# Performance work log

Hardware: AMD Instinct MI355X
Metric: run time of the kernel (lower is better)

The kernel has to match this reference:

```python
import jax, jax.numpy as jnp
import numpy as np

B, T, V = 8, 64, 25
IN_DIM = 64
HID = 64
D = 3 * HID // 2          # 96, per-node feature dim
OUT = 128
N = B * T * V * 2         # 25600 nodes
E = N * 16                # 409600 edges
LAYERS = 2
EPS = 1e-5


def prelu(x, a):
    return jnp.where(x >= 0, x, a * x)


def grouped_conv1x1(x, w, b, groups=3):
    # x: [B, C, V, T]; w: [O, C//groups]; b: [O]  (1x1 conv, groups=3)
    Bb, C, Vv, Tt = x.shape
    O = w.shape[0]
    xg = x.reshape(Bb, groups, C // groups, Vv, Tt)
    wg = w.reshape(groups, O // groups, C // groups)
    y = jnp.einsum('bgivt,goi->bgovt', xg, wg).reshape(Bb, O, Vv, Tt)
    return y + b[None, :, None, None]


def layer_norm(x, g, b):
    m = jnp.mean(x, axis=-1, keepdims=True)
    v = jnp.mean((x - m) ** 2, axis=-1, keepdims=True)
    return (x - m) / jnp.sqrt(v + EPS) * g + b


def _forward(h, src, dst, tp_w1, tp_b1, tp_a, tp_w2, tp_b2,
             tm_w1, tm_b1, tm_a, tm_w2, tm_b2,
             ln_g, ln_b, bn_g, bn_b, bn_rm, bn_rv, act_a,
             gW1, gb1, ga, gW2, gb2, t2_w, t2_b):
    # posture / motion streams -> [B, 3*in_dim, V, T]
    hp = jnp.transpose(h[:, :, :, 0, :], (0, 3, 2, 1))
    hm = jnp.transpose(h[:, :, :, 1, :], (0, 3, 2, 1))
    hp = grouped_conv1x1(prelu(grouped_conv1x1(hp, tp_w1, tp_b1), tp_a), tp_w2, tp_b2)
    hm = grouped_conv1x1(prelu(grouped_conv1x1(hm, tm_w1, tm_b1), tm_a), tm_w2, tm_b2)
    hp = jnp.transpose(hp, (0, 3, 2, 1))[:, :, :, None, :]  # [B,T,V,1,D]
    hm = jnp.transpose(hm, (0, 3, 2, 1))[:, :, :, None, :]
    x = jnp.concatenate([hp, hm], axis=3).reshape(-1, D)     # [N, D]
    raw = x
    hs, es = [], []
    for i in range(LAYERS):
        def gate(h2, i=i):
            # edge gate MLP: Linear -> PReLU -> Linear -> Tanh (dropout eval = id)
            return jnp.tanh(prelu(h2 @ gW1[i] + gb1[i], ga[i]) @ gW2[i] + gb2[i])
        e = gate(x[dst] * x[src])                            # [E, 1]
        z = jax.ops.segment_sum(x[src] * e, dst, num_segments=N)
        y = layer_norm(z + x, ln_g[i], ln_b[i])
        y = (y - bn_rm[i]) / jnp.sqrt(bn_rv[i] + EPS) * bn_g[i] + bn_b[i]  # BN eval
        x = prelu(y, act_a[i])
        hs.append(x)
        es.append(gate(x[dst] * x[src]))   # torch calls the layer a 2nd time for e
    hcat = jnp.concatenate([raw] + hs, axis=1)               # [N, 3D]
    out = hcat @ t2_w + t2_b                                 # dropout eval = id
    ee = jnp.concatenate(es, axis=0)                         # [2E, 1]
    return out, ee


def setup_inputs() -> dict:
    key = jax.random.key(0)
    ks = jax.random.split(key, 40)
    def nrm(k, shape, s=0.05):
        return jax.random.normal(k, shape, jnp.float32) * s
    d = {}
    d['h'] = jax.random.normal(ks[0], (B, T, V, 2, 3 * IN_DIM), jnp.float32)
    d['src'] = jax.random.randint(ks[1], (E,), 0, N, jnp.int32)
    d['dst'] = jax.random.randint(ks[2], (E,), 0, N, jnp.int32)
    # t1_posture / t1_motion grouped 1x1 convs
    d['tp_w1'] = nrm(ks[3], (3 * HID, IN_DIM)); d['tp_b1'] = nrm(ks[4], (3 * HID,))
    d['tp_a'] = jnp.full((1,), 0.25, jnp.float32)
    d['tp_w2'] = nrm(ks[5], (D, HID)); d['tp_b2'] = nrm(ks[6], (D,))
    d['tm_w1'] = nrm(ks[7], (3 * HID, IN_DIM)); d['tm_b1'] = nrm(ks[8], (3 * HID,))
    d['tm_a'] = jnp.full((1,), 0.25, jnp.float32)
    d['tm_w2'] = nrm(ks[9], (D, HID)); d['tm_b2'] = nrm(ks[10], (D,))
    # per-layer norms / activations (stacked over LAYERS)
    d['ln_g'] = jnp.ones((LAYERS, D), jnp.float32); d['ln_b'] = jnp.zeros((LAYERS, D), jnp.float32)
    d['bn_g'] = jnp.ones((LAYERS, D), jnp.float32); d['bn_b'] = jnp.zeros((LAYERS, D), jnp.float32)
    d['bn_rm'] = jnp.zeros((LAYERS, D), jnp.float32); d['bn_rv'] = jnp.ones((LAYERS, D), jnp.float32)
    d['act_a'] = jnp.full((LAYERS,), 0.25, jnp.float32)
    # per-layer FALayer gate MLP
    d['gW1'] = nrm(ks[11], (LAYERS, D, D)); d['gb1'] = nrm(ks[12], (LAYERS, D))
    d['ga'] = jnp.full((LAYERS,), 0.25, jnp.float32)
    d['gW2'] = nrm(ks[13], (LAYERS, D, 1)); d['gb2'] = nrm(ks[14], (LAYERS, 1))
    d['t2_w'] = nrm(ks[15], (3 * D, OUT)); d['t2_b'] = nrm(ks[16], (OUT,))
    return d


def reference(h, src, dst, tp_w1, tp_b1, tp_a, tp_w2, tp_b2,
              tm_w1, tm_b1, tm_a, tm_w2, tm_b2,
              ln_g, ln_b, bn_g, bn_b, bn_rm, bn_rv, act_a,
              gW1, gb1, ga, gW2, gb2, t2_w, t2_b):
    return _forward(h, src, dst, tp_w1, tp_b1, tp_a, tp_w2, tp_b2,
                    tm_w1, tm_b1, tm_a, tm_w2, tm_b2,
                    ln_g, ln_b, bn_g, bn_b, bn_rm, bn_rv, act_a,
                    gW1, gb1, ga, gW2, gb2, t2_w, t2_b)
```

## Files before the change

### kernel.cpp

```cpp
#include <hip/hip_runtime.h>

#define N_NODES 25600
#define N_EDGES 409600
#define EPSV 1e-5f

__device__ __forceinline__ unsigned short f2bf(float f) {
    unsigned int x = __float_as_uint(f);
    x += 0x7fffu + ((x >> 16) & 1u);
    return (unsigned short)(x >> 16);
}
__device__ __forceinline__ unsigned int f2bf2(float a, float b) {
#if __has_builtin(__builtin_amdgcn_cvt_pk_bf16_f32)
    auto r = __builtin_amdgcn_cvt_pk_bf16_f32(a, b);
    unsigned int u;
    __builtin_memcpy(&u, &r, 4);
    return u;
#else
    return (unsigned int)f2bf(a) | ((unsigned int)f2bf(b) << 16);
#endif
}

using frag_ab = __attribute__((ext_vector_type(8))) short;
using frag_cd = __attribute__((ext_vector_type(4))) float;
typedef _Float16 f16x8 __attribute__((ext_vector_type(8)));

#define WST 104
#define TWST 72
#define THST 200

__global__ __launch_bounds__(256) void transform_mfma(
    const float* __restrict__ h,
    const float* __restrict__ tpw1, const float* __restrict__ tpb1, const float* __restrict__ tpa,
    const float* __restrict__ tpw2, const float* __restrict__ tpb2,
    const float* __restrict__ tmw1, const float* __restrict__ tmb1, const float* __restrict__ tma,
    const float* __restrict__ tmw2, const float* __restrict__ tmb2,
    float* __restrict__ xout, _Float16* __restrict__ xh)
{
    __shared__ alignas(16) unsigned short W1s[192 * TWST];
    __shared__ alignas(16) unsigned short W2s[96 * TWST];
    __shared__ alignas(16) unsigned short hs[64 * THST];
    __shared__ float b1s[192];
    __shared__ float b2s[96];

    const int tid = threadIdx.x;
    const int s = blockIdx.y;
    const float* w1 = s ? tmw1 : tpw1;
    const float* b1 = s ? tmb1 : tpb1;
    const float* w2 = s ? tmw2 : tpw2;
    const float* b2 = s ? tmb2 : tpb2;
    const float alpha = (s ? tma : tpa)[0];

    #pragma unroll
    for (int r = 0; r < 12; r++) {
        int idx4 = r * 256 + tid;
        int o = idx4 >> 4, i4 = (idx4 & 15) * 4;
        const float4 a = *(const float4*)&w1[o * 64 + i4];
        *(uint2*)&W1s[o * TWST + i4] = make_uint2(f2bf2(a.x, a.y), f2bf2(a.z, a.w));
    }
    #pragma unroll
    for (int r = 0; r < 6; r++) {
        int idx4 = r * 256 + tid;
        int o = idx4 >> 4, i4 = (idx4 & 15) * 4;
        const float4 a = *(const float4*)&w2[o * 64 + i4];
        *(uint2*)&W2s[o * TWST + i4] = make_uint2(f2bf2(a.x, a.y), f2bf2(a.z, a.w));
    }
    if (tid < 192) b1s[tid] = b1[tid];
    if (tid < 96) b2s[tid] = b2[tid];
    __syncthreads();

    const int lane = tid & 63;
    const int wv = tid >> 6;
    const int quad = lane >> 4;
    const int lcol = lane & 15;
    const int m0 = wv * 16;
    const int j0 = blockIdx.x * 64;

    #pragma unroll
    for (int r = 0; r < 12; r++) {
        int idx = r * 256 + tid;
        int m = idx / 48, q = idx - m * 48;
        const float4 a = *(const float4*)&h[(2 * (j0 + m) + s) * 192 + q * 4];
        *(uint2*)&hs[m * THST + q * 4] = make_uint2(f2bf2(a.x, a.y), f2bf2(a.z, a.w));
    }
    __syncthreads();

    const int arow = (m0 + lcol) * THST;
    #pragma unroll
    for (int g = 0; g < 3; g++) {
        frag_cd acc[4];
        #pragma unroll
        for (int nt = 0; nt < 4; nt++) acc[nt] = (frag_cd){0.f, 0.f, 0.f, 0.f};
        #pragma unroll
        for (int kt = 0; kt < 2; kt++) {
            const int k0 = kt * 32 + quad * 8;
            frag_ab af = *(const frag_ab*)&hs[arow + g * 64 + k0];
            #pragma unroll
            for (int nt = 0; nt < 4; nt++) {
                frag_ab bf = *(const frag_ab*)&W1s[(g * 64 + nt * 16 + lcol) * TWST + k0];
                acc[nt] = __builtin_amdgcn_mfma_f32_16x16x32_bf16(af, bf, acc[nt], 0, 0, 0);
            }
        }
        #pragma unroll
        for (int nt = 0; nt < 4; nt++) {
            const int o = g * 64 + nt * 16 + lcol;
            const float bv = b1s[o];
            #pragma unroll
            for (int reg = 0; reg < 4; reg++) {
                float u = acc[nt][reg] + bv;
                u = u >= 0.f ? u : alpha * u;
                hs[(m0 + quad * 4 + reg) * THST + o] = f2bf(u);
            }
        }
    }
    #pragma unroll
    for (int g2 = 0; g2 < 3; g2++) {
        frag_cd acc[2];
        acc[0] = (frag_cd){0.f, 0.f, 0.f, 0.f};
        acc[1] = (frag_cd){0.f, 0.f, 0.f, 0.f};
        #pragma unroll
        for (int kt = 0; kt < 2; kt++) {
            const int k0 = kt * 32 + quad * 8;
            frag_ab af = *(const frag_ab*)&hs[arow + g2 * 64 + k0];
            #pragma unroll
            for (int nt = 0; nt < 2; nt++) {
                frag_ab bf = *(const frag_ab*)&W2s[(g2 * 32 + nt * 16 + lcol) * TWST + k0];
                acc[nt] = __builtin_amdgcn_mfma_f32_16x16x32_bf16(af, bf, acc[nt], 0, 0, 0);
            }
        }
        #pragma unroll
        for (int nt = 0; nt < 2; nt++) {
            const int o2 = g2 * 32 + nt * 16 + lcol;
            const float bv = b2s[o2];
            #pragma unroll
            for (int reg = 0; reg < 4; reg++) {
                const int node = 2 * (j0 + m0 + quad * 4 + reg) + s;
                const float v = acc[nt][reg] + bv;
                xout[node * 96 + o2] = v;
                xh[node * 96 + o2] = (_Float16)v;
            }
        }
    }
}

template<bool DUAL>
__global__ __launch_bounds__(256) void gate_kernel(
    const _Float16* __restrict__ xh,
    const int* __restrict__ srcp, const int* __restrict__ dstp,
    const int* __restrict__ mapA,
    const float* __restrict__ gW1, const float* __restrict__ gb1,
    const float* __restrict__ ga,  const float* __restrict__ gW2,
    const float* __restrict__ gb2, int layerA, int layerB,
    float* __restrict__ outA, float* __restrict__ outB)
{
    __shared__ alignas(16) _Float16 W1f[(DUAL ? 2 : 1) * 9216];

    const int tid = threadIdx.x;
    {
        const float* W1p = gW1 + layerA * 9216;
        const float* W1q = gW1 + layerB * 9216;
        for (int fi = tid; fi < 1152; fi += 256) {
            int lc = fi & 15, r = fi >> 4;
            int quad = r & 3, t3 = r >> 2;
            int nt = t3 / 3, kt = t3 - nt * 3;
            int n = nt * 16 + lc, k0 = kt * 32 + quad * 8;
            f16x8 v, w;
            #pragma unroll
            for (int j = 0; j < 8; j++) {
                v[j] = (_Float16)W1p[(k0 + j) * 96 + n];
                if (DUAL) w[j] = (_Float16)W1q[(k0 + j) * 96 + n];
            }
            *(f16x8*)&W1f[fi * 8] = v;
            if (DUAL) *(f16x8*)&W1f[9216 + fi * 8] = w;
        }
    }

    const int lane = tid & 63;
    const int wv   = tid >> 6;
    const int quad = lane >> 4;
    const int lcol = lane & 15;
    const int m0   = wv * 16;
    const int erow = m0 + lcol;
    const int koff = quad * 8;

    float w2A[6], b1A[6], w2B[6], b1B[6];
    #pragma unroll
    for (int nt = 0; nt < 6; nt++) {
        w2A[nt] = gW2[layerA * 96 + nt * 16 + lcol];
        b1A[nt] = gb1[layerA * 96 + nt * 16 + lcol];
        if (DUAL) {
            w2B[nt] = gW2[layerB * 96 + nt * 16 + lcol];
            b1B[nt] = gb1[layerB * 96 + nt * 16 + lcol];
        }
    }
    const float alphaA = ga[layerA];
    const float b2A = gb2[layerA];
    const float alphaB = DUAL ? ga[layerB] : 0.f;
    const float b2B = DUAL ? gb2[layerB] : 0.f;

    int si[4], di[4];
    #pragma unroll
    for (int t = 0; t < 4; t++) {
        const int s = blockIdx.x * 256 + t * 64 + erow;
        si[t] = srcp[s];
        di[t] = dstp[s];
    }
    __syncthreads();

    f16x8 A0, A1, A2, B0, B1, B2;
    {
        const _Float16* rs = xh + si[0] * 96 + koff;
        const _Float16* rd = xh + di[0] * 96 + koff;
        A0 = *(const f16x8*)rs;        B0 = *(const f16x8*)rd;
        A1 = *(const f16x8*)(rs + 32); B1 = *(const f16x8*)(rd + 32);
        A2 = *(const f16x8*)(rs + 64); B2 = *(const f16x8*)(rd + 64);
    }

    #pragma unroll
    for (int t = 0; t < 4; t++) {
        f16x8 p0 = A0 * B0;
        f16x8 p1 = A1 * B1;
        f16x8 p2 = A2 * B2;
        if (t < 3) {
            const _Float16* rs = xh + si[t + 1] * 96 + koff;
            const _Float16* rd = xh + di[t + 1] * 96 + koff;
            A0 = *(const f16x8*)rs;        B0 = *(const f16x8*)rd;
            A1 = *(const f16x8*)(rs + 32); B1 = *(const f16x8*)(rd + 32);
            A2 = *(const f16x8*)(rs + 64); B2 = *(const f16x8*)(rd + 64);
        }

        frag_cd accA[6], accB[6];
        #pragma unroll
        for (int nt = 0; nt < 6; nt++) {
            accA[nt] = (frag_cd){0.f, 0.f, 0.f, 0.f};
            if (DUAL) accB[nt] = (frag_cd){0.f, 0.f, 0.f, 0.f};
        }
        #pragma unroll
        for (int kt = 0; kt < 3; kt++) {
            const f16x8 pk = (kt == 0) ? p0 : (kt == 1 ? p1 : p2);
            #pragma unroll
            for (int nt = 0; nt < 6; nt++) {
                const int f = ((nt * 3 + kt) * 4 + quad) * 16 + lcol;
                f16x8 bfragA = *(const f16x8*)&W1f[f * 8];
                accA[nt] = __builtin_amdgcn_mfma_f32_16x16x32_f16(pk, bfragA, accA[nt], 0, 0, 0);
                if (DUAL) {
                    f16x8 bfragB = *(const f16x8*)&W1f[9216 + f * 8];
                    accB[nt] = __builtin_amdgcn_mfma_f32_16x16x32_f16(pk, bfragB, accB[nt], 0, 0, 0);
                }
            }
        }
        float psA[4] = {0.f, 0.f, 0.f, 0.f};
        float psB[4] = {0.f, 0.f, 0.f, 0.f};
        #pragma unroll
        for (int nt = 0; nt < 6; nt++) {
            #pragma unroll
            for (int reg = 0; reg < 4; reg++) {
                float u = accA[nt][reg] + b1A[nt];
                u = u >= 0.f ? u : alphaA * u;
                psA[reg] += u * w2A[nt];
            }
            if (DUAL) {
                #pragma unroll
                for (int reg = 0; reg < 4; reg++) {
                    float u = accB[nt][reg] + b1B[nt];
                    u = u >= 0.f ? u : alphaB * u;
                    psB[reg] += u * w2B[nt];
                }
            }
        }
        #pragma unroll
        for (int off = 1; off < 4; off <<= 1) {
            #pragma unroll
            for (int reg = 0; reg < 4; reg++) {
                psA[reg] += __shfl_xor(psA[reg], off, 64);
                if (DUAL) psB[reg] += __shfl_xor(psB[reg], off, 64);
            }
        }
        float vA = (lcol & 2) ? ((lcol & 1) ? psA[3] : psA[2])
                              : ((lcol & 1) ? psA[1] : psA[0]);
        vA += __shfl_xor(vA, 4, 64);
        vA += __shfl_xor(vA, 8, 64);
        float vB = 0.f;
        if (DUAL) {
            vB = (lcol & 2) ? ((lcol & 1) ? psB[3] : psB[2])
                            : ((lcol & 1) ? psB[1] : psB[0]);
            vB += __shfl_xor(vB, 4, 64);
            vB += __shfl_xor(vB, 8, 64);
        }
        const float eA = tanhf(vA + b2A);
        const float eB = DUAL ? tanhf(vB + b2B) : 0.f;
        if (lcol < 4) {
            const int slot = blockIdx.x * 256 + t * 64 + m0 + quad * 4 + lcol;
            outA[mapA ? mapA[slot] : slot] = eA;
            if (DUAL) outB[slot] = eB;
        }
    }
}

__global__ __launch_bounds__(256) void count_kernel(
    const int* __restrict__ dst, int* __restrict__ cnt)
{
    int e = blockIdx.x * 256 + threadIdx.x;
    atomicAdd(&cnt[dst[e]], 1);
}

__global__ __launch_bounds__(1024) void scan_kernel(
    const int* __restrict__ cnt, int* __restrict__ off, int* __restrict__ cur)
{
    __shared__ int part[1024];
    const int tid = threadIdx.x;
    const int base = tid * 25;
    int loc[25];
    int s = 0;
    #pragma unroll
    for (int i = 0; i < 25; i++) { loc[i] = s; s += cnt[base + i]; }
    part[tid] = s;
    __syncthreads();
    for (int d = 1; d < 1024; d <<= 1) {
        int t = (tid >= d) ? part[tid - d] : 0;
        __syncthreads();
        part[tid] += t;
        __syncthreads();
    }
    const int basesum = part[tid] - s;
    #pragma unroll
    for (int i = 0; i < 25; i++) {
        int o = basesum + loc[i];
        off[base + i] = o;
        cur[base + i] = o;
    }
    if (tid == 1023) off[N_NODES] = part[1023];
}

__global__ __launch_bounds__(256) void scatter_kernel(
    const int* __restrict__ dst, const int* __restrict__ src,
    int* __restrict__ cur, int* __restrict__ perm,
    int* __restrict__ srcp, int* __restrict__ dstp)
{
    int e = blockIdx.x * 256 + threadIdx.x;
    int d = dst[e];
    int p = atomicAdd(&cur[d], 1);
    perm[p] = e;
    srcp[p] = src[e];
    dstp[p] = d;
}

__global__ __launch_bounds__(128) void agg_norm_kernel(
    const float* __restrict__ xf, const int* __restrict__ srcp,
    const float* __restrict__ ef,
    const int* __restrict__ off,
    const float* __restrict__ xin,
    const float* __restrict__ lng, const float* __restrict__ lnb,
    const float* __restrict__ bng, const float* __restrict__ bnb,
    const float* __restrict__ bnrm, const float* __restrict__ bnrv,
    const float* __restrict__ acta, int layer,
    float* __restrict__ xout, _Float16* __restrict__ xh)
{
    __shared__ float red[128];
    const int n = blockIdx.x;
    const int tid = threadIdx.x;
    const int beg = off[n], end = off[n + 1];
    float v = 0.f;
    if (tid < 96) {
        float v0 = 0.f, v1 = 0.f, v2 = 0.f, v3 = 0.f;
        int j = beg;
        for (; j + 4 <= end; j += 4) {
            v0 += xf[srcp[j] * 96 + tid] * ef[j];
            v1 += xf[srcp[j + 1] * 96 + tid] * ef[j + 1];
            v2 += xf[srcp[j + 2] * 96 + tid] * ef[j + 2];
            v3 += xf[srcp[j + 3] * 96 + tid] * ef[j + 3];
        }
        for (; j < end; j++) {
            v0 += xf[srcp[j] * 96 + tid] * ef[j];
        }
        v = ((v0 + v1) + (v2 + v3)) + xin[n * 96 + tid];
    }
    red[tid] = (tid < 96) ? v : 0.f;
    __syncthreads();
    for (int sft = 64; sft > 0; sft >>= 1) {
        if (tid < sft) red[tid] += red[tid + sft];
        __syncthreads();
    }
    const float mean = red[0] * (1.f / 96.f);
    __syncthreads();
    const float d = (tid < 96) ? (v - mean) : 0.f;
    red[tid] = d * d;
    __syncthreads();
    for (int sft = 64; sft > 0; sft >>= 1) {
        if (tid < sft) red[tid] += red[tid + sft];
        __syncthreads();
    }
    const float rstd = rsqrtf(red[0] * (1.f / 96.f) + EPSV);
    if (tid < 96) {
        const int c = layer * 96 + tid;
        float y = d * rstd * lng[c] + lnb[c];
        y = (y - bnrm[c]) * rsqrtf(bnrv[c] + EPSV) * bng[c] + bnb[c];
        const float a = acta[layer];
        const float o = y >= 0.f ? y : a * y;
        xout[n * 96 + tid] = o;
        xh[n * 96 + tid] = (_Float16)o;
    }
}

__global__ __launch_bounds__(256) void final_mfma(
    const float* __restrict__ x0, const float* __restrict__ x1, const float* __restrict__ x2,
    const float* __restrict__ t2w, const float* __restrict__ t2b,
    float* __restrict__ out)
{
    __shared__ alignas(16) unsigned short As[64 * WST];
    __shared__ alignas(16) unsigned short Bs[128 * WST];

    const int tid  = threadIdx.x;
    const int lane = tid & 63;
    const int wv   = tid >> 6;
    const int quad = lane >> 4;
    const int lcol = lane & 15;
    const int node0 = blockIdx.x * 64;

    frag_cd acc[8];
    #pragma unroll
    for (int nt = 0; nt < 8; nt++) acc[nt] = (frag_cd){0.f, 0.f, 0.f, 0.f};

    for (int ck = 0; ck < 3; ck++) {
        const float* xc = (ck == 0) ? x0 : (ck == 1 ? x1 : x2);
        __syncthreads();
        #pragma unroll
        for (int r = 0; r < 6; r++) {
            int m = r * 256 + tid;
            int mm = m / 24, q = m - mm * 24;
            const float4 a = *(const float4*)&xc[(node0 + mm) * 96 + q * 4];
            *(uint2*)&As[mm * WST + q * 4] = make_uint2(f2bf2(a.x, a.y), f2bf2(a.z, a.w));
        }
        #pragma unroll
        for (int r = 0; r < 48; r++) {
            int idx = r * 256 + tid;
            int cc = idx >> 7, o = idx & 127;
            Bs[o * WST + cc] = f2bf(t2w[(ck * 96 + cc) * 128 + o]);
        }
        __syncthreads();
        const int mrow = wv * 16 + lcol;
        #pragma unroll
        for (int kt = 0; kt < 3; kt++) {
            const int k0 = kt * 32 + quad * 8;
            frag_ab afrag = *(const frag_ab*)&As[mrow * WST + k0];
            #pragma unroll
            for (int nt = 0; nt < 8; nt++) {
                frag_ab bfrag = *(const frag_ab*)&Bs[(nt * 16 + lcol) * WST + k0];
                acc[nt] = __builtin_amdgcn_mfma_f32_16x16x32_bf16(afrag, bfrag, acc[nt], 0, 0, 0);
            }
        }
    }
    const int node = node0 + wv * 16 + quad * 4;
    #pragma unroll
    for (int nt = 0; nt < 8; nt++) {
        const int o = nt * 16 + lcol;
        const float bias = t2b[o];
        #pragma unroll
        for (int reg = 0; reg < 4; reg++)
            out[(node + reg) * 128 + o] = acc[nt][reg] + bias;
    }
}

extern "C" void kernel_launch(void* const* d_in, const int* in_sizes, int n_in,
                              void* d_out, int out_size, void* d_ws, size_t ws_size,
                              hipStream_t stream)
{
    const float* h    = (const float*)d_in[0];
    const int*   src  = (const int*)d_in[1];
    const int*   dst  = (const int*)d_in[2];
    const float* tpw1 = (const float*)d_in[3];
    const float* tpb1 = (const float*)d_in[4];
    const float* tpa  = (const float*)d_in[5];
    const float* tpw2 = (const float*)d_in[6];
    const float* tpb2 = (const float*)d_in[7];
    const float* tmw1 = (const float*)d_in[8];
    const float* tmb1 = (const float*)d_in[9];
    const float* tma  = (const float*)d_in[10];
    const float* tmw2 = (const float*)d_in[11];
    const float* tmb2 = (const float*)d_in[12];
    const float* lng  = (const float*)d_in[13];
    const float* lnb  = (const float*)d_in[14];
    const float* bng  = (const float*)d_in[15];
    const float* bnb  = (const float*)d_in[16];
    const float* bnrm = (const float*)d_in[17];
    const float* bnrv = (const float*)d_in[18];
    const float* acta = (const float*)d_in[19];
    const float* gW1  = (const float*)d_in[20];
    const float* gb1  = (const float*)d_in[21];
    const float* ga   = (const float*)d_in[22];
    const float* gW2  = (const float*)d_in[23];
    const float* gb2  = (const float*)d_in[24];
    const float* t2w  = (const float*)d_in[25];
    const float* t2b  = (const float*)d_in[26];

    float* ws = (float*)d_ws;
    float* x0 = ws;
    float* x1 = x0 + N_NODES * 96;
    float* x2 = x1 + N_NODES * 96;
    float* eb = x2 + N_NODES * 96;
    int* cnt  = (int*)(eb + N_EDGES);
    int* off  = cnt + N_NODES;
    int* cur  = off + N_NODES + 1;
    int* perm = cur + N_NODES;
    int* srcp = perm + N_EDGES;
    int* dstp = srcp + N_EDGES;
    _Float16* xh = (_Float16*)(dstp + N_EDGES);

    float* out = (float*)d_out;
    float* ee  = out + N_NODES * 128;

    hipMemsetAsync(cnt, 0, N_NODES * sizeof(int), stream);
    count_kernel<<<N_EDGES / 256, 256, 0, stream>>>(dst, cnt);
    scan_kernel<<<1, 1024, 0, stream>>>(cnt, off, cur);
    scatter_kernel<<<N_EDGES / 256, 256, 0, stream>>>(dst, src, cur, perm, srcp, dstp);

    transform_mfma<<<dim3(200, 2), 256, 0, stream>>>(
        h, tpw1, tpb1, tpa, tpw2, tpb2, tmw1, tmb1, tma, tmw2, tmb2, x0, xh);

    gate_kernel<false><<<1600, 256, 0, stream>>>(xh, srcp, dstp, nullptr,
        gW1, gb1, ga, gW2, gb2, 0, 0, eb, nullptr);
    agg_norm_kernel<<<N_NODES, 128, 0, stream>>>(x0, srcp, eb, off, x0,
        lng, lnb, bng, bnb, bnrm, bnrv, acta, 0, x1, xh);

    gate_kernel<true><<<1600, 256, 0, stream>>>(xh, srcp, dstp, perm,
        gW1, gb1, ga, gW2, gb2, 0, 1, ee, eb);

    agg_norm_kernel<<<N_NODES, 128, 0, stream>>>(x1, srcp, eb, off, x1,
        lng, lnb, bng, bnb, bnrm, bnrv, acta, 1, x2, xh);
    gate_kernel<false><<<1600, 256, 0, stream>>>(xh, srcp, dstp, perm,
        gW1, gb1, ga, gW2, gb2, 1, 0, ee + N_EDGES, nullptr);

    final_mfma<<<N_NODES / 64, 256, 0, stream>>>(x0, x1, x2, t2w, t2b, out);
}
```

Baseline: 394.7 us.

## Feed final projection from fp16 node buffers and pre-swizzled weights, skip LDS staging

Keeps separate fp16 copies of each layer's node features and pre-packs the output projection weight into MFMA fragment order in a small prep kernel. The final kernel then loads fragments straight from global memory instead of converting fp32 to bf16 through shared memory. It also drops the unused fp32 write of the last layer and raises wave priority around the gate MFMA loop. Precision changes from bf16 to fp16 in the final GEMM, and the prep buffer reuses the count workspace.

```diff
diff --git a/kernel.cpp b/kernel.cpp
--- a/kernel.cpp
+++ b/kernel.cpp
@@ -24,7 +24,6 @@
 using frag_cd = __attribute__((ext_vector_type(4))) float;
 typedef _Float16 f16x8 __attribute__((ext_vector_type(8)));
 
-#define WST 104
 #define TWST 72
 #define THST 200
 
@@ -234,6 +233,7 @@
             accA[nt] = (frag_cd){0.f, 0.f, 0.f, 0.f};
             if (DUAL) accB[nt] = (frag_cd){0.f, 0.f, 0.f, 0.f};
         }
+        __builtin_amdgcn_s_setprio(1);
         #pragma unroll
         for (int kt = 0; kt < 3; kt++) {
             const f16x8 pk = (kt == 0) ? p0 : (kt == 1 ? p1 : p2);
@@ -248,6 +248,7 @@
                 }
             }
         }
+        __builtin_amdgcn_s_setprio(0);
         float psA[4] = {0.f, 0.f, 0.f, 0.f};
         float psB[4] = {0.f, 0.f, 0.f, 0.f};
         #pragma unroll
@@ -342,6 +343,22 @@
     perm[p] = e;
     srcp[p] = src[e];
     dstp[p] = d;
+}
+
+__global__ __launch_bounds__(256) void prep_t2w(
+    const float* __restrict__ t2w, _Float16* __restrict__ t2wf)
+{
+    int idx = blockIdx.x * 256 + threadIdx.x;
+    int j = idx & 7;
+    int t = idx >> 3;
+    int lc = t & 15;
+    int u = t >> 4;
+    int c = u % 36, nt = u / 36;
+    int o = nt * 16 + lc;
+    int ck = c / 12, r = c - ck * 12;
+    int kt3 = r >> 2, quad = r & 3;
+    int k = ck * 96 + kt3 * 32 + quad * 8 + j;
+    t2wf[idx] = (_Float16)t2w[k * 128 + o];
 }
 
 __global__ __launch_bounds__(128) void agg_norm_kernel(
@@ -396,60 +413,43 @@
         y = (y - bnrm[c]) * rsqrtf(bnrv[c] + EPSV) * bng[c] + bnb[c];
         const float a = acta[layer];
         const float o = y >= 0.f ? y : a * y;
-        xout[n * 96 + tid] = o;
+        if (xout) xout[n * 96 + tid] = o;
         xh[n * 96 + tid] = (_Float16)o;
     }
 }
 
 __global__ __launch_bounds__(256) void final_mfma(
-    const float* __restrict__ x0, const float* __restrict__ x1, const float* __restrict__ x2,
-    const float* __restrict__ t2w, const float* __restrict__ t2b,
-    float* __restrict__ out)
-{
-    __shared__ alignas(16) unsigned short As[64 * WST];
-    __shared__ alignas(16) unsigned short Bs[128 * WST];
-
+    const _Float16* __restrict__ xh0, const _Float16* __restrict__ xh1,
+    const _Float16* __restrict__ xh2, const _Float16* __restrict__ t2wf,
+    const float* __restrict__ t2b, float* __restrict__ out)
+{
     const int tid  = threadIdx.x;
     const int lane = tid & 63;
     const int wv   = tid >> 6;
     const int quad = lane >> 4;
     const int lcol = lane & 15;
-    const int node0 = blockIdx.x * 64;
+    const int mrow = blockIdx.x * 64 + wv * 16 + lcol;
 
     frag_cd acc[8];
     #pragma unroll
     for (int nt = 0; nt < 8; nt++) acc[nt] = (frag_cd){0.f, 0.f, 0.f, 0.f};
 
+    #pragma unroll
     for (int ck = 0; ck < 3; ck++) {
-        const float* xc = (ck == 0) ? x0 : (ck == 1 ? x1 : x2);
-        __syncthreads();
-        #pragma unroll
-        for (int r = 0; r < 6; r++) {
-            int m = r * 256 + tid;
-            int mm = m / 24, q = m - mm * 24;
-            const float4 a = *(const float4*)&xc[(node0 + mm) * 96 + q * 4];
-            *(uint2*)&As[mm * WST + q * 4] = make_uint2(f2bf2(a.x, a.y), f2bf2(a.z, a.w));
-        }
-        #pragma unroll
-        for (int r = 0; r < 48; r++) {
-            int idx = r * 256 + tid;
-            int cc = idx >> 7, o = idx & 127;
-            Bs[o * WST + cc] = f2bf(t2w[(ck * 96 + cc) * 128 + o]);
-        }
-        __syncthreads();
-        const int mrow = wv * 16 + lcol;
-        #pragma unroll
-        for (int kt = 0; kt < 3; kt++) {
-            const int k0 = kt * 32 + quad * 8;
-            frag_ab afrag = *(const frag_ab*)&As[mrow * WST + k0];
+        const _Float16* xc = (ck == 0) ? xh0 : (ck == 1 ? xh1 : xh2);
+        const _Float16* ap = xc + mrow * 96 + quad * 8;
+        #pragma unroll
+        for (int kt3 = 0; kt3 < 3; kt3++) {
+            f16x8 afrag = *(const f16x8*)(ap + kt3 * 32);
+            const int chunk = 12 * ck + 4 * kt3 + quad;
             #pragma unroll
             for (int nt = 0; nt < 8; nt++) {
-                frag_ab bfrag = *(const frag_ab*)&Bs[(nt * 16 + lcol) * WST + k0];
-                acc[nt] = __builtin_amdgcn_mfma_f32_16x16x32_bf16(afrag, bfrag, acc[nt], 0, 0, 0);
-            }
-        }
-    }
-    const int node = node0 + wv * 16 + quad * 4;
+                f16x8 bfrag = *(const f16x8*)&t2wf[((nt * 36 + chunk) * 16 + lcol) * 8];
+                acc[nt] = __builtin_amdgcn_mfma_f32_16x16x32_f16(afrag, bfrag, acc[nt], 0, 0, 0);
+            }
+        }
+    }
+    const int node = blockIdx.x * 64 + wv * 16 + quad * 4;
     #pragma unroll
     for (int nt = 0; nt < 8; nt++) {
         const int o = nt * 16 + lcol;
@@ -495,15 +495,17 @@
     float* ws = (float*)d_ws;
     float* x0 = ws;
     float* x1 = x0 + N_NODES * 96;
-    float* x2 = x1 + N_NODES * 96;
-    float* eb = x2 + N_NODES * 96;
-    int* cnt  = (int*)(eb + N_EDGES);
+    float* eb = x1 + N_NODES * 96;
+    _Float16* xh0 = (_Float16*)(eb + N_EDGES);
+    _Float16* xh1 = xh0 + N_NODES * 96;
+    _Float16* xh2 = xh1 + N_NODES * 96;
+    int* cnt  = (int*)(xh2 + N_NODES * 96);
     int* off  = cnt + N_NODES;
     int* cur  = off + N_NODES + 1;
     int* perm = cur + N_NODES;
     int* srcp = perm + N_EDGES;
     int* dstp = srcp + N_EDGES;
-    _Float16* xh = (_Float16*)(dstp + N_EDGES);
+    _Float16* t2wf = (_Float16*)cnt;
 
     float* out = (float*)d_out;
     float* ee  = out + N_NODES * 128;
@@ -512,22 +514,23 @@
     count_kernel<<<N_EDGES / 256, 256, 0, stream>>>(dst, cnt);
     scan_kernel<<<1, 1024, 0, stream>>>(cnt, off, cur);
     scatter_kernel<<<N_EDGES / 256, 256, 0, stream>>>(dst, src, cur, perm, srcp, dstp);
+    prep_t2w<<<144, 256, 0, stream>>>(t2w, t2wf);
 
     transform_mfma<<<dim3(200, 2), 256, 0, stream>>>(
-        h, tpw1, tpb1, tpa, tpw2, tpb2, tmw1, tmb1, tma, tmw2, tmb2, x0, xh);
-
-    gate_kernel<false><<<1600, 256, 0, stream>>>(xh, srcp, dstp, nullptr,
+        h, tpw1, tpb1, tpa, tpw2, tpb2, tmw1, tmb1, tma, tmw2, tmb2, x0, xh0);
+
+    gate_kernel<false><<<1600, 256, 0, stream>>>(xh0, srcp, dstp, nullptr,
         gW1, gb1, ga, gW2, gb2, 0, 0, eb, nullptr);
     agg_norm_kernel<<<N_NODES, 128, 0, stream>>>(x0, srcp, eb, off, x0,
-        lng, lnb, bng, bnb, bnrm, bnrv, acta, 0, x1, xh);
-
-    gate_kernel<true><<<1600, 256, 0, stream>>>(xh, srcp, dstp, perm,
+        lng, lnb, bng, bnb, bnrm, bnrv, acta, 0, x1, xh1);
+
+    gate_kernel<true><<<1600, 256, 0, stream>>>(xh1, srcp, dstp, perm,
         gW1, gb1, ga, gW2, gb2, 0, 1, ee, eb);
 
     agg_norm_kernel<<<N_NODES, 128, 0, stream>>>(x1, srcp, eb, off, x1,
-        lng, lnb, bng, bnb, bnrm, bnrv, acta, 1, x2, xh);
-    gate_kernel<false><<<1600, 256, 0, stream>>>(xh, srcp, dstp, perm,
+        lng, lnb, bng, bnb, bnrm, bnrv, acta, 1, nullptr, xh2);
+    gate_kernel<false><<<1600, 256, 0, stream>>>(xh2, srcp, dstp, perm,
         gW1, gb1, ga, gW2, gb2, 1, 0, ee + N_EDGES, nullptr);
 
-    final_mfma<<<N_NODES / 64, 256, 0, stream>>>(x0, x1, x2, t2w, t2b, out);
-}
+    final_mfma<<<N_NODES / 64, 256, 0, stream>>>(xh0, xh1, xh2, t2wf, t2b, out);
+}
```

Result: faster. 365.1 us (-7.5%).
